# Kernel optimization log

Measured on AMD Instinct MI355X. Metric: run time of the kernel, lower is better.

The kernel has to match this reference:

```python
import jax, jax.numpy as jnp
import numpy as np


def setup_inputs() -> dict:
    key = jax.random.key(0)
    k1, k2, k3 = jax.random.split(key, 3)
    shape = (8, 2, 1024, 1024)
    predict = jax.random.normal(k1, shape, dtype=jnp.float32)
    target = jax.random.normal(k2, shape, dtype=jnp.float32)
    weight = jax.random.uniform(k3, shape, dtype=jnp.float32)
    return {"predict": predict, "target": target, "weight": weight, "min_kept": 2000000}


def reference(predict, target, weight, min_kept):
    # norm_term = prod(spatial dims) * batch  (channels NOT included, per source)
    B = predict.shape[0]
    spatial = float(np.prod(predict.shape[2:]))
    norm_term = jnp.float32(spatial * B)

    sq = (predict - target) ** 2
    loss_flat = (sq / norm_term).reshape(-1)          # unweighted per-elem MSE
    # threshold = sorted_ascending[N - min_kept] == min_kept-th largest value.
    # top_k replaces the full sort (same order statistic, ties identical).
    topk_vals, _ = jax.lax.top_k(loss_flat, min_kept)
    threshold = topk_vals[min_kept - 1]

    wloss_flat = (weight * sq / norm_term).reshape(-1)
    mask = loss_flat > threshold                      # strict >, as in source
    cnt = jnp.sum(mask)
    # reduction == 'elementwise_mean': mean over selected elements
    return jnp.sum(jnp.where(mask, wloss_flat, 0.0)) / cnt.astype(wloss_flat.dtype)
```

## Files before the change

### kernel.cpp

```cpp
#include <hip/hip_runtime.h>
#include <stdint.h>


#define H2_BITS 17
#define H1_SIZE 32768
#define H1_WORDS (H1_SIZE / 2)
#define H2_SIZE 131072
#define SHARDS 64

#define OFF_H2   262144
#define OFF_META 786432
#define OFF_SUMS 786496
#define OFF_SHC  786560
#define OFF_CAND 786944

__device__ __forceinline__ void hist_add4(uint32_t* lh, float4 pv, float4 tv) {
    float d0 = pv.x - tv.x, d1 = pv.y - tv.y, d2 = pv.z - tv.z, d3 = pv.w - tv.w;
    uint32_t b0 = __float_as_uint(d0 * d0 * 0x1p-23f) >> H2_BITS;
    uint32_t b1 = __float_as_uint(d1 * d1 * 0x1p-23f) >> H2_BITS;
    uint32_t b2 = __float_as_uint(d2 * d2 * 0x1p-23f) >> H2_BITS;
    uint32_t b3 = __float_as_uint(d3 * d3 * 0x1p-23f) >> H2_BITS;
    atomicAdd(&lh[b0 >> 1], 1u << ((b0 & 1) * 16));
    atomicAdd(&lh[b1 >> 1], 1u << ((b1 & 1) * 16));
    atomicAdd(&lh[b2 >> 1], 1u << ((b2 & 1) * 16));
    atomicAdd(&lh[b3 >> 1], 1u << ((b3 & 1) * 16));
}

__global__ __launch_bounds__(1024) void k_hist1(
    const float4* __restrict__ p, const float4* __restrict__ t,
    uint32_t* __restrict__ hist1, int n4)
{
    __shared__ uint32_t lh[H1_WORDS];
    for (int j = threadIdx.x; j < H1_WORDS; j += 1024) lh[j] = 0;
    __syncthreads();
    const int S = gridDim.x * 1024;
    int i = blockIdx.x * 1024 + threadIdx.x;
    for (; i + 3 * S < n4; i += 4 * S) {
        float4 pv0 = p[i],         tv0 = t[i];
        float4 pv1 = p[i + S],     tv1 = t[i + S];
        float4 pv2 = p[i + 2 * S], tv2 = t[i + 2 * S];
        float4 pv3 = p[i + 3 * S], tv3 = t[i + 3 * S];
        hist_add4(lh, pv0, tv0);
        hist_add4(lh, pv1, tv1);
        hist_add4(lh, pv2, tv2);
        hist_add4(lh, pv3, tv3);
    }
    for (; i < n4; i += S) hist_add4(lh, p[i], t[i]);
    __syncthreads();
    uint32_t* dst = hist1 + (blockIdx.x & 1) * H1_SIZE;
    const uint32_t rot = (blockIdx.x >> 1) * 64;
    for (int jj = threadIdx.x; jj < H1_WORDS; jj += 1024) {
        int j = (int)((jj + rot) & (H1_WORDS - 1));
        uint32_t v = lh[j];
        uint32_t c0 = v & 0xFFFFu, c1 = v >> 16;
        if (c0) atomicAdd(&dst[2 * j], c0);
        if (c1) atomicAdd(&dst[2 * j + 1], c1);
    }
}

__global__ __launch_bounds__(1024) void k_scan1(
    const uint32_t* __restrict__ hist1, const int* __restrict__ min_kept,
    uint32_t* __restrict__ meta)
{
    __shared__ uint32_t psum[1024];
    __shared__ uint32_t gsuf[64];
    const int t = threadIdx.x;
    const uint32_t k = (uint32_t)(*min_kept);
    const uint32_t* h0 = hist1;
    const uint32_t* h1 = hist1 + H1_SIZE;
    const int per = H1_SIZE / 1024;
    const int base = t * per;
    uint32_t s = 0;
    #pragma unroll
    for (int i = 0; i < per; i++) s += h0[base + i] + h1[base + i];
    psum[t] = s;
    __syncthreads();
    if (t < 64) {
        uint32_t g = 0;
        for (int i = 0; i < 16; i++) g += psum[t * 16 + i];
        uint32_t v = g;
        #pragma unroll
        for (int off = 1; off < 64; off <<= 1) {
            uint32_t o = __shfl_down(v, off);
            if (t + off < 64) v += o;
        }
        gsuf[t] = v;
    }
    __syncthreads();
    const int g = t >> 4;
    uint32_t cum = (g < 63) ? gsuf[g + 1] : 0;
    const int gend = g * 16 + 15;
    for (int j = t + 1; j <= gend; j++) cum += psum[j];
    if (cum < k && k <= cum + psum[t]) {
        uint32_t c = cum;
        for (int i = per - 1; i >= 0; i--) {
            uint32_t h = h0[base + i] + h1[base + i];
            c += h;
            if (c >= k) {
                meta[0] = (uint32_t)(base + i);
                meta[1] = k - (c - h);
                break;
            }
        }
    }
}

__global__ __launch_bounds__(256) void k_main(
    const float4* __restrict__ p, const float4* __restrict__ t,
    const float4* __restrict__ w,
    uint32_t* meta, uint32_t* __restrict__ hist2,
    double* __restrict__ sums, uint32_t* __restrict__ shard_cnt,
    uint2* __restrict__ cand, uint32_t cap_per_shard, int n4)
{
    const uint32_t b = meta[0];
    double lsum = 0.0;
    uint32_t lcnt = 0;
    const int shard = blockIdx.x & (SHARDS - 1);
    uint32_t* my_cnt = &shard_cnt[shard];
    uint2* my_cand = cand + (size_t)shard * cap_per_shard;
    const int lane = threadIdx.x & 63;

    auto proc = [&](float4 pv, float4 tv, float4 wv) {
        float d[4] = {pv.x - tv.x, pv.y - tv.y, pv.z - tv.z, pv.w - tv.w};
        float wa[4] = {wv.x, wv.y, wv.z, wv.w};
        #pragma unroll
        for (int c = 0; c < 4; c++) {
            float loss = d[c] * d[c] * 0x1p-23f;
            uint32_t bits = __float_as_uint(loss);
            uint32_t hi = bits >> H2_BITS;
            if (hi > b) {
                lcnt++;
                lsum += (double)(wa[c] * loss);
            }
            unsigned long long m = __ballot(hi == b);
            if (m) {
                if (hi == b) {
                    int pos = __popcll(m & ((1ull << lane) - 1ull));
                    int leader = __ffsll(m) - 1;
                    uint32_t base_ = 0;
                    if (lane == leader)
                        base_ = atomicAdd(my_cnt, (uint32_t)__popcll(m));
                    base_ = __shfl(base_, leader);
                    uint32_t idx = base_ + (uint32_t)pos;
                    if (idx < cap_per_shard)
                        my_cand[idx] = make_uint2(bits, __float_as_uint(wa[c]));
                    else
                        meta[3] = 1u;
                    atomicAdd(&hist2[bits & (H2_SIZE - 1)], 1u);
                }
            }
        }
    };

    const int S = gridDim.x * 256;
    int i = blockIdx.x * 256 + threadIdx.x;
    for (; i + S < n4; i += 2 * S) {
        float4 pv0 = p[i],     tv0 = t[i],     wv0 = w[i];
        float4 pv1 = p[i + S], tv1 = t[i + S], wv1 = w[i + S];
        proc(pv0, tv0, wv0);
        proc(pv1, tv1, wv1);
    }
    for (; i < n4; i += S) proc(p[i], t[i], w[i]);

    #pragma unroll
    for (int off = 32; off; off >>= 1) {
        lsum += __shfl_down(lsum, off);
        lcnt += __shfl_down(lcnt, off);
    }
    __shared__ double sred[4];
    __shared__ uint32_t cred[4];
    const int wid = threadIdx.x >> 6;
    if (lane == 0) { sred[wid] = lsum; cred[wid] = lcnt; }
    __syncthreads();
    if (threadIdx.x == 0) {
        double bs = sred[0] + sred[1] + sred[2] + sred[3];
        uint32_t bc = cred[0] + cred[1] + cred[2] + cred[3];
        atomicAdd(&sums[0], bs);
        atomicAdd(&meta[4], bc);
    }
}

__global__ __launch_bounds__(1024) void k_scan2(
    const uint32_t* __restrict__ hist2, uint32_t* meta)
{
    __shared__ uint32_t psum[1024];
    __shared__ uint32_t gsuf[64];
    const int t = threadIdx.x;
    const uint32_t k = meta[1];
    const uint32_t b = meta[0];
    const int per = H2_SIZE / 1024;
    const int base = t * per;
    uint32_t s = 0;
    for (int i = 0; i < per; i++) s += hist2[base + i];
    psum[t] = s;
    __syncthreads();
    if (t < 64) {
        uint32_t g = 0;
        for (int i = 0; i < 16; i++) g += psum[t * 16 + i];
        uint32_t v = g;
        #pragma unroll
        for (int off = 1; off < 64; off <<= 1) {
            uint32_t o = __shfl_down(v, off);
            if (t + off < 64) v += o;
        }
        gsuf[t] = v;
    }
    __syncthreads();
    const int g = t >> 4;
    uint32_t cum = (g < 63) ? gsuf[g + 1] : 0;
    const int gend = g * 16 + 15;
    for (int j = t + 1; j <= gend; j++) cum += psum[j];
    if (cum < k && k <= cum + psum[t]) {
        uint32_t c = cum;
        for (int i = per - 1; i >= 0; i--) {
            uint32_t h = hist2[base + i];
            c += h;
            if (c >= k) {
                meta[2] = (b << H2_BITS) | (uint32_t)(base + i);
                break;
            }
        }
    }
}

__global__ __launch_bounds__(256) void k_cand(
    const float4* __restrict__ p, const float4* __restrict__ t,
    const float4* __restrict__ w,
    uint32_t* meta, const uint32_t* __restrict__ shard_cnt,
    const uint2* __restrict__ cand, uint32_t cap_per_shard,
    double* __restrict__ sums, int n4)
{
    const uint32_t thr = meta[2];
    const uint32_t overflow = meta[3];
    double lsum = 0.0;
    uint32_t lcnt = 0;
    if (!overflow) {
        for (int sdx = 0; sdx < SHARDS; sdx++) {
            uint32_t cnt = shard_cnt[sdx];
            if (cnt > cap_per_shard) cnt = cap_per_shard;
            const uint2* cs = cand + (size_t)sdx * cap_per_shard;
            for (uint32_t i = blockIdx.x * 256 + threadIdx.x; i < cnt;
                 i += gridDim.x * 256) {
                uint2 e = cs[i];
                if (e.x > thr) {
                    lcnt++;
                    lsum += (double)(__uint_as_float(e.y) * __uint_as_float(e.x));
                }
            }
        }
    } else {
        const uint32_t bb = meta[0];
        const int S = gridDim.x * 256;
        for (int i = blockIdx.x * 256 + threadIdx.x; i < n4; i += S) {
            float4 pv = p[i], tv = t[i], wv = w[i];
            float d[4] = {pv.x - tv.x, pv.y - tv.y, pv.z - tv.z, pv.w - tv.w};
            float wa[4] = {wv.x, wv.y, wv.z, wv.w};
            #pragma unroll
            for (int c = 0; c < 4; c++) {
                float loss = d[c] * d[c] * 0x1p-23f;
                uint32_t bits = __float_as_uint(loss);
                if ((bits >> H2_BITS) == bb && bits > thr) {
                    lcnt++;
                    lsum += (double)(wa[c] * loss);
                }
            }
        }
    }
    #pragma unroll
    for (int off = 32; off; off >>= 1) {
        lsum += __shfl_down(lsum, off);
        lcnt += __shfl_down(lcnt, off);
    }
    __shared__ double sred[4];
    __shared__ uint32_t cred[4];
    const int wid = threadIdx.x >> 6, lane = threadIdx.x & 63;
    if (lane == 0) { sred[wid] = lsum; cred[wid] = lcnt; }
    __syncthreads();
    if (threadIdx.x == 0) {
        double bs = sred[0] + sred[1] + sred[2] + sred[3];
        uint32_t bc = cred[0] + cred[1] + cred[2] + cred[3];
        atomicAdd(&sums[1], bs);
        atomicAdd(&meta[5], bc);
    }
}

__global__ __launch_bounds__(64) void k_final(
    const double* __restrict__ sums, const uint32_t* __restrict__ meta,
    float* __restrict__ out)
{
    if (threadIdx.x == 0 && blockIdx.x == 0) {
        double s = sums[0] + sums[1];
        double c = (double)(meta[4] + meta[5]);
        out[0] = (float)(s / c);
    }
}

extern "C" void kernel_launch(void* const* d_in, const int* in_sizes, int n_in,
                              void* d_out, int out_size, void* d_ws, size_t ws_size,
                              hipStream_t stream) {
    const float* p = (const float*)d_in[0];
    const float* t = (const float*)d_in[1];
    const float* w = (const float*)d_in[2];
    const int* mk = (const int*)d_in[3];
    float* out = (float*)d_out;
    const int n = in_sizes[0];
    const int n4 = n / 4;

    uint8_t* ws = (uint8_t*)d_ws;
    uint32_t* hist1 = (uint32_t*)ws;
    uint32_t* hist2 = (uint32_t*)(ws + OFF_H2);
    uint32_t* meta  = (uint32_t*)(ws + OFF_META);
    double*   sums  = (double*)(ws + OFF_SUMS);
    uint32_t* shcnt = (uint32_t*)(ws + OFF_SHC);
    uint2*    cand  = (uint2*)(ws + OFF_CAND);
    uint32_t cap_per_shard = 0;
    if (ws_size > OFF_CAND + SHARDS * 8) {
        cap_per_shard = (uint32_t)((ws_size - OFF_CAND) / (8 * SHARDS));
    }

    hipMemsetAsync(d_ws, 0, OFF_CAND, stream);
    k_hist1<<<512, 1024, 0, stream>>>((const float4*)p, (const float4*)t, hist1, n4);
    k_scan1<<<1, 1024, 0, stream>>>(hist1, mk, meta);
    k_main<<<2048, 256, 0, stream>>>((const float4*)p, (const float4*)t,
                                     (const float4*)w, meta, hist2, sums, shcnt,
                                     cand, cap_per_shard, n4);
    k_scan2<<<1, 1024, 0, stream>>>(hist2, meta);
    k_cand<<<256, 256, 0, stream>>>((const float4*)p, (const float4*)t,
                                    (const float4*)w, meta, shcnt, cand,
                                    cap_per_shard, sums, n4);
    k_final<<<1, 64, 0, stream>>>(sums, meta, out);
}
```

Baseline: 386.1 us.

## Software-pipeline streaming loads and move hist2 build into separate candidate kernel

The histogram and main passes switch from grid-stride loops to fixed contiguous chunks per block (8192 and 4096 float4s). Loads are explicitly pipelined ahead of compute, with scheduling barriers keeping several loads in flight. The main kernel drops the per-wave ballot and the sharded candidate counters in favour of one global atomic counter per candidate element. Building the second-level histogram moves into a new small kernel that reads the candidate list, so the main streaming pass does less atomic work. In exchange it adds a kernel launch and risks contention on the single global counter if many elements fall in the threshold bucket.

```diff
diff --git a/kernel.cpp b/kernel.cpp
--- a/kernel.cpp
+++ b/kernel.cpp
@@ -6,13 +6,13 @@
 #define H1_SIZE 32768
 #define H1_WORDS (H1_SIZE / 2)
 #define H2_SIZE 131072
-#define SHARDS 64
 
 #define OFF_H2   262144
 #define OFF_META 786432
 #define OFF_SUMS 786496
-#define OFF_SHC  786560
-#define OFF_CAND 786944
+#define OFF_CAND 786560
+
+#define SB() __builtin_amdgcn_sched_barrier(0)
 
 __device__ __forceinline__ void hist_add4(uint32_t* lh, float4 pv, float4 tv) {
     float d0 = pv.x - tv.x, d1 = pv.y - tv.y, d2 = pv.z - tv.z, d3 = pv.w - tv.w;
@@ -33,19 +33,26 @@
     __shared__ uint32_t lh[H1_WORDS];
     for (int j = threadIdx.x; j < H1_WORDS; j += 1024) lh[j] = 0;
     __syncthreads();
-    const int S = gridDim.x * 1024;
-    int i = blockIdx.x * 1024 + threadIdx.x;
-    for (; i + 3 * S < n4; i += 4 * S) {
-        float4 pv0 = p[i],         tv0 = t[i];
-        float4 pv1 = p[i + S],     tv1 = t[i + S];
-        float4 pv2 = p[i + 2 * S], tv2 = t[i + 2 * S];
-        float4 pv3 = p[i + 3 * S], tv3 = t[i + 3 * S];
-        hist_add4(lh, pv0, tv0);
-        hist_add4(lh, pv1, tv1);
-        hist_add4(lh, pv2, tv2);
-        hist_add4(lh, pv3, tv3);
-    }
-    for (; i < n4; i += S) hist_add4(lh, p[i], t[i]);
+    const int tid = threadIdx.x;
+    const int base = blockIdx.x * 8192;
+    if (base + 8192 <= n4) {
+        const float4* pb = p + base;
+        const float4* tb = t + base;
+#define H1LD(u) float4 P##u = pb[tid + (u)*1024]; float4 T##u = tb[tid + (u)*1024];
+#define H1PR(u) hist_add4(lh, P##u, T##u);
+        H1LD(0) H1LD(1) H1LD(2)
+        SB();
+        H1LD(3) SB(); H1PR(0)
+        H1LD(4) SB(); H1PR(1)
+        H1LD(5) SB(); H1PR(2)
+        H1LD(6) SB(); H1PR(3)
+        H1LD(7) SB(); H1PR(4)
+        H1PR(5) H1PR(6) H1PR(7)
+#undef H1LD
+#undef H1PR
+    } else {
+        for (int i = base + tid; i < n4; i += 1024) hist_add4(lh, p[i], t[i]);
+    }
     __syncthreads();
     uint32_t* dst = hist1 + (blockIdx.x & 1) * H1_SIZE;
     const uint32_t rot = (blockIdx.x >> 1) * 64;
@@ -107,60 +114,66 @@
 
 __global__ __launch_bounds__(256) void k_main(
     const float4* __restrict__ p, const float4* __restrict__ t,
-    const float4* __restrict__ w,
-    uint32_t* meta, uint32_t* __restrict__ hist2,
-    double* __restrict__ sums, uint32_t* __restrict__ shard_cnt,
-    uint2* __restrict__ cand, uint32_t cap_per_shard, int n4)
+    const float4* __restrict__ w, uint32_t* meta,
+    double* __restrict__ sums, uint2* __restrict__ cand,
+    uint32_t cap, int n4)
 {
     const uint32_t b = meta[0];
     double lsum = 0.0;
     uint32_t lcnt = 0;
-    const int shard = blockIdx.x & (SHARDS - 1);
-    uint32_t* my_cnt = &shard_cnt[shard];
-    uint2* my_cand = cand + (size_t)shard * cap_per_shard;
-    const int lane = threadIdx.x & 63;
+    const int tid = threadIdx.x;
+    const int base = blockIdx.x * 4096;
 
     auto proc = [&](float4 pv, float4 tv, float4 wv) {
-        float d[4] = {pv.x - tv.x, pv.y - tv.y, pv.z - tv.z, pv.w - tv.w};
+        float d0 = pv.x - tv.x, d1 = pv.y - tv.y, d2 = pv.z - tv.z, d3 = pv.w - tv.w;
+        float l0 = d0 * d0 * 0x1p-23f, l1 = d1 * d1 * 0x1p-23f;
+        float l2 = d2 * d2 * 0x1p-23f, l3 = d3 * d3 * 0x1p-23f;
         float wa[4] = {wv.x, wv.y, wv.z, wv.w};
+        float lo[4] = {l0, l1, l2, l3};
         #pragma unroll
         for (int c = 0; c < 4; c++) {
-            float loss = d[c] * d[c] * 0x1p-23f;
-            uint32_t bits = __float_as_uint(loss);
+            uint32_t bits = __float_as_uint(lo[c]);
             uint32_t hi = bits >> H2_BITS;
-            if (hi > b) {
-                lcnt++;
-                lsum += (double)(wa[c] * loss);
-            }
-            unsigned long long m = __ballot(hi == b);
-            if (m) {
-                if (hi == b) {
-                    int pos = __popcll(m & ((1ull << lane) - 1ull));
-                    int leader = __ffsll(m) - 1;
-                    uint32_t base_ = 0;
-                    if (lane == leader)
-                        base_ = atomicAdd(my_cnt, (uint32_t)__popcll(m));
-                    base_ = __shfl(base_, leader);
-                    uint32_t idx = base_ + (uint32_t)pos;
-                    if (idx < cap_per_shard)
-                        my_cand[idx] = make_uint2(bits, __float_as_uint(wa[c]));
-                    else
-                        meta[3] = 1u;
-                    atomicAdd(&hist2[bits & (H2_SIZE - 1)], 1u);
-                }
+            bool above = hi > b;
+            lcnt += above ? 1u : 0u;
+            lsum += above ? (double)(wa[c] * lo[c]) : 0.0;
+            if (hi == b) {
+                uint32_t idx = atomicAdd(&meta[6], 1u);
+                if (idx < cap) cand[idx] = make_uint2(bits, __float_as_uint(wa[c]));
+                else meta[3] = 1u;
             }
         }
     };
 
-    const int S = gridDim.x * 256;
-    int i = blockIdx.x * 256 + threadIdx.x;
-    for (; i + S < n4; i += 2 * S) {
-        float4 pv0 = p[i],     tv0 = t[i],     wv0 = w[i];
-        float4 pv1 = p[i + S], tv1 = t[i + S], wv1 = w[i + S];
-        proc(pv0, tv0, wv0);
-        proc(pv1, tv1, wv1);
-    }
-    for (; i < n4; i += S) proc(p[i], t[i], w[i]);
+    if (base + 4096 <= n4) {
+        const float4* pb = p + base;
+        const float4* tb = t + base;
+        const float4* wb = w + base;
+#define MLD(u) float4 P##u = pb[tid + (u)*256]; float4 T##u = tb[tid + (u)*256]; \
+               float4 W##u = wb[tid + (u)*256];
+#define MPR(u) proc(P##u, T##u, W##u);
+        MLD(0) MLD(1)
+        SB();
+        MLD(2)  SB(); MPR(0)
+        MLD(3)  SB(); MPR(1)
+        MLD(4)  SB(); MPR(2)
+        MLD(5)  SB(); MPR(3)
+        MLD(6)  SB(); MPR(4)
+        MLD(7)  SB(); MPR(5)
+        MLD(8)  SB(); MPR(6)
+        MLD(9)  SB(); MPR(7)
+        MLD(10) SB(); MPR(8)
+        MLD(11) SB(); MPR(9)
+        MLD(12) SB(); MPR(10)
+        MLD(13) SB(); MPR(11)
+        MLD(14) SB(); MPR(12)
+        MLD(15) SB(); MPR(13)
+        MPR(14) MPR(15)
+#undef MLD
+#undef MPR
+    } else {
+        for (int i = base + tid; i < n4; i += 256) proc(p[i], t[i], w[i]);
+    }
 
     #pragma unroll
     for (int off = 32; off; off >>= 1) {
@@ -169,7 +182,7 @@
     }
     __shared__ double sred[4];
     __shared__ uint32_t cred[4];
-    const int wid = threadIdx.x >> 6;
+    const int wid = threadIdx.x >> 6, lane = threadIdx.x & 63;
     if (lane == 0) { sred[wid] = lsum; cred[wid] = lcnt; }
     __syncthreads();
     if (threadIdx.x == 0) {
@@ -177,6 +190,34 @@
         uint32_t bc = cred[0] + cred[1] + cred[2] + cred[3];
         atomicAdd(&sums[0], bs);
         atomicAdd(&meta[4], bc);
+    }
+}
+
+__global__ __launch_bounds__(256) void k_hist2b(
+    const float4* __restrict__ p, const float4* __restrict__ t,
+    uint32_t* __restrict__ meta, const uint2* __restrict__ cand,
+    uint32_t cap, uint32_t* __restrict__ hist2, int n4)
+{
+    if (!meta[3]) {
+        uint32_t cnt = meta[6];
+        if (cnt > cap) cnt = cap;
+        for (uint32_t i = blockIdx.x * 256 + threadIdx.x; i < cnt;
+             i += gridDim.x * 256) {
+            atomicAdd(&hist2[cand[i].x & (H2_SIZE - 1)], 1u);
+        }
+    } else {
+        const uint32_t b = meta[0];
+        const int S = gridDim.x * 256;
+        for (int i = blockIdx.x * 256 + threadIdx.x; i < n4; i += S) {
+            float4 pv = p[i], tv = t[i];
+            float d[4] = {pv.x - tv.x, pv.y - tv.y, pv.z - tv.z, pv.w - tv.w};
+            #pragma unroll
+            for (int c = 0; c < 4; c++) {
+                uint32_t bits = __float_as_uint(d[c] * d[c] * 0x1p-23f);
+                if ((bits >> H2_BITS) == b)
+                    atomicAdd(&hist2[bits & (H2_SIZE - 1)], 1u);
+            }
+        }
     }
 }
 
@@ -225,9 +266,8 @@
 
 __global__ __launch_bounds__(256) void k_cand(
     const float4* __restrict__ p, const float4* __restrict__ t,
-    const float4* __restrict__ w,
-    uint32_t* meta, const uint32_t* __restrict__ shard_cnt,
-    const uint2* __restrict__ cand, uint32_t cap_per_shard,
+    const float4* __restrict__ w, uint32_t* meta,
+    const uint2* __restrict__ cand, uint32_t cap,
     double* __restrict__ sums, int n4)
 {
     const uint32_t thr = meta[2];
@@ -235,17 +275,14 @@
     double lsum = 0.0;
     uint32_t lcnt = 0;
     if (!overflow) {
-        for (int sdx = 0; sdx < SHARDS; sdx++) {
-            uint32_t cnt = shard_cnt[sdx];
-            if (cnt > cap_per_shard) cnt = cap_per_shard;
-            const uint2* cs = cand + (size_t)sdx * cap_per_shard;
-            for (uint32_t i = blockIdx.x * 256 + threadIdx.x; i < cnt;
-                 i += gridDim.x * 256) {
-                uint2 e = cs[i];
-                if (e.x > thr) {
-                    lcnt++;
-                    lsum += (double)(__uint_as_float(e.y) * __uint_as_float(e.x));
-                }
+        uint32_t cnt = meta[6];
+        if (cnt > cap) cnt = cap;
+        for (uint32_t i = blockIdx.x * 256 + threadIdx.x; i < cnt;
+             i += gridDim.x * 256) {
+            uint2 e = cand[i];
+            if (e.x > thr) {
+                lcnt++;
+                lsum += (double)(__uint_as_float(e.y) * __uint_as_float(e.x));
             }
         }
     } else {
@@ -311,22 +348,23 @@
     uint32_t* hist2 = (uint32_t*)(ws + OFF_H2);
     uint32_t* meta  = (uint32_t*)(ws + OFF_META);
     double*   sums  = (double*)(ws + OFF_SUMS);
-    uint32_t* shcnt = (uint32_t*)(ws + OFF_SHC);
     uint2*    cand  = (uint2*)(ws + OFF_CAND);
-    uint32_t cap_per_shard = 0;
-    if (ws_size > OFF_CAND + SHARDS * 8) {
-        cap_per_shard = (uint32_t)((ws_size - OFF_CAND) / (8 * SHARDS));
+    uint32_t cap = 0;
+    if (ws_size > OFF_CAND + 8) {
+        cap = (uint32_t)((ws_size - OFF_CAND) / 8);
     }
 
     hipMemsetAsync(d_ws, 0, OFF_CAND, stream);
-    k_hist1<<<512, 1024, 0, stream>>>((const float4*)p, (const float4*)t, hist1, n4);
+    const int nb1 = (n4 + 8191) / 8192;
+    const int nbm = (n4 + 4095) / 4096;
+    k_hist1<<<nb1, 1024, 0, stream>>>((const float4*)p, (const float4*)t, hist1, n4);
     k_scan1<<<1, 1024, 0, stream>>>(hist1, mk, meta);
-    k_main<<<2048, 256, 0, stream>>>((const float4*)p, (const float4*)t,
-                                     (const float4*)w, meta, hist2, sums, shcnt,
-                                     cand, cap_per_shard, n4);
+    k_main<<<nbm, 256, 0, stream>>>((const float4*)p, (const float4*)t,
+                                    (const float4*)w, meta, sums, cand, cap, n4);
+    k_hist2b<<<32, 256, 0, stream>>>((const float4*)p, (const float4*)t,
+                                     meta, cand, cap, hist2, n4);
     k_scan2<<<1, 1024, 0, stream>>>(hist2, meta);
-    k_cand<<<256, 256, 0, stream>>>((const float4*)p, (const float4*)t,
-                                    (const float4*)w, meta, shcnt, cand,
-                                    cap_per_shard, sums, n4);
+    k_cand<<<64, 256, 0, stream>>>((const float4*)p, (const float4*)t,
+                                   (const float4*)w, meta, cand, cap, sums, n4);
     k_final<<<1, 64, 0, stream>>>(sums, meta, out);
 }
```

Result: slower. 681.4 us (+76.5%).

## Replace full-pass histogram with sampled bounds and candidate-window selection

Applied to the files above, without the earlier changes.

Replaces the full first-pass histogram over predict/target with a small strided sample (64 blocks, 2 chunks per wave) that estimates a bin window bracketing the k-th largest loss. The main pass then accumulates elements above the window and collects in-window candidates, and later histogram/scan stages run only on those candidates. A fallback path redoes full histograms over the data if the window guess is wrong or the buffer overflows. The 1/norm scale is dropped from the per-element loss and applied once at the end. This removes one full read of two inputs but adds several small serial kernel launches.

```diff
diff --git a/kernel.cpp b/kernel.cpp
--- a/kernel.cpp
+++ b/kernel.cpp
@@ -2,77 +2,70 @@
 #include <stdint.h>
 
 
-#define H2_BITS 17
-#define H1_SIZE 32768
-#define H1_WORDS (H1_SIZE / 2)
+#define BIN_SHIFT 17
+#define NBINS 32768
+#define NB_WORDS (NBINS / 2)
+#define WMAX 4096
 #define H2_SIZE 131072
 #define SHARDS 64
 
-#define OFF_H2   262144
-#define OFF_META 786432
-#define OFF_SUMS 786496
-#define OFF_SHC  786560
-#define OFF_CAND 786944
+#define OFF_WIN   131072u
+#define OFF_H2    147456u
+#define OFF_FULL  671744u
+#define OFF_META  802816u
+#define OFF_SUMS  802944u
+#define OFF_SHC   802976u
+#define OFF_CAND  803232u
 
 __device__ __forceinline__ void hist_add4(uint32_t* lh, float4 pv, float4 tv) {
     float d0 = pv.x - tv.x, d1 = pv.y - tv.y, d2 = pv.z - tv.z, d3 = pv.w - tv.w;
-    uint32_t b0 = __float_as_uint(d0 * d0 * 0x1p-23f) >> H2_BITS;
-    uint32_t b1 = __float_as_uint(d1 * d1 * 0x1p-23f) >> H2_BITS;
-    uint32_t b2 = __float_as_uint(d2 * d2 * 0x1p-23f) >> H2_BITS;
-    uint32_t b3 = __float_as_uint(d3 * d3 * 0x1p-23f) >> H2_BITS;
+    uint32_t b0 = __float_as_uint(d0 * d0) >> BIN_SHIFT;
+    uint32_t b1 = __float_as_uint(d1 * d1) >> BIN_SHIFT;
+    uint32_t b2 = __float_as_uint(d2 * d2) >> BIN_SHIFT;
+    uint32_t b3 = __float_as_uint(d3 * d3) >> BIN_SHIFT;
     atomicAdd(&lh[b0 >> 1], 1u << ((b0 & 1) * 16));
     atomicAdd(&lh[b1 >> 1], 1u << ((b1 & 1) * 16));
     atomicAdd(&lh[b2 >> 1], 1u << ((b2 & 1) * 16));
     atomicAdd(&lh[b3 >> 1], 1u << ((b3 & 1) * 16));
 }
 
-__global__ __launch_bounds__(1024) void k_hist1(
+__global__ __launch_bounds__(256) void k_sample(
     const float4* __restrict__ p, const float4* __restrict__ t,
-    uint32_t* __restrict__ hist1, int n4)
-{
-    __shared__ uint32_t lh[H1_WORDS];
-    for (int j = threadIdx.x; j < H1_WORDS; j += 1024) lh[j] = 0;
-    __syncthreads();
-    const int S = gridDim.x * 1024;
-    int i = blockIdx.x * 1024 + threadIdx.x;
-    for (; i + 3 * S < n4; i += 4 * S) {
-        float4 pv0 = p[i],         tv0 = t[i];
-        float4 pv1 = p[i + S],     tv1 = t[i + S];
-        float4 pv2 = p[i + 2 * S], tv2 = t[i + 2 * S];
-        float4 pv3 = p[i + 3 * S], tv3 = t[i + 3 * S];
-        hist_add4(lh, pv0, tv0);
-        hist_add4(lh, pv1, tv1);
-        hist_add4(lh, pv2, tv2);
-        hist_add4(lh, pv3, tv3);
-    }
-    for (; i < n4; i += S) hist_add4(lh, p[i], t[i]);
-    __syncthreads();
-    uint32_t* dst = hist1 + (blockIdx.x & 1) * H1_SIZE;
-    const uint32_t rot = (blockIdx.x >> 1) * 64;
-    for (int jj = threadIdx.x; jj < H1_WORDS; jj += 1024) {
-        int j = (int)((jj + rot) & (H1_WORDS - 1));
+    uint32_t* __restrict__ shist, int n4, int chunk_stride)
+{
+    __shared__ uint32_t lh[NB_WORDS];
+    for (int j = threadIdx.x; j < NB_WORDS; j += 256) lh[j] = 0;
+    __syncthreads();
+    const int gw = blockIdx.x * 4 + (threadIdx.x >> 6);
+    const int lane = threadIdx.x & 63;
+    #pragma unroll
+    for (int c = 0; c < 2; c++) {
+        int ch = gw * 2 + c;
+        int idx = ch * chunk_stride + lane;
+        if (idx < n4) hist_add4(lh, p[idx], t[idx]);
+    }
+    __syncthreads();
+    for (int j = threadIdx.x; j < NB_WORDS; j += 256) {
         uint32_t v = lh[j];
         uint32_t c0 = v & 0xFFFFu, c1 = v >> 16;
-        if (c0) atomicAdd(&dst[2 * j], c0);
-        if (c1) atomicAdd(&dst[2 * j + 1], c1);
-    }
-}
-
-__global__ __launch_bounds__(1024) void k_scan1(
-    const uint32_t* __restrict__ hist1, const int* __restrict__ min_kept,
-    uint32_t* __restrict__ meta)
+        if (c0) atomicAdd(&shist[2 * j], c0);
+        if (c1) atomicAdd(&shist[2 * j + 1], c1);
+    }
+}
+
+__global__ __launch_bounds__(1024) void k_bounds(
+    const uint32_t* __restrict__ shist, const int* __restrict__ mk,
+    uint32_t* __restrict__ meta, uint32_t inv)
 {
     __shared__ uint32_t psum[1024];
     __shared__ uint32_t gsuf[64];
+    __shared__ uint32_t sBh, sBlp1;
     const int t = threadIdx.x;
-    const uint32_t k = (uint32_t)(*min_kept);
-    const uint32_t* h0 = hist1;
-    const uint32_t* h1 = hist1 + H1_SIZE;
-    const int per = H1_SIZE / 1024;
+    if (t == 0) { sBh = 0xFFFFFFFFu; sBlp1 = 0u; }
+    const int per = NBINS / 1024;
     const int base = t * per;
     uint32_t s = 0;
-    #pragma unroll
-    for (int i = 0; i < per; i++) s += h0[base + i] + h1[base + i];
+    for (int i = 0; i < per; i++) s += shist[base + i];
     psum[t] = s;
     __syncthreads();
     if (t < 64) {
@@ -91,62 +84,83 @@
     uint32_t cum = (g < 63) ? gsuf[g + 1] : 0;
     const int gend = g * 16 + 15;
     for (int j = t + 1; j <= gend; j++) cum += psum[j];
-    if (cum < k && k <= cum + psum[t]) {
-        uint32_t c = cum;
-        for (int i = per - 1; i >= 0; i--) {
-            uint32_t h = h0[base + i] + h1[base + i];
-            c += h;
-            if (c >= k) {
-                meta[0] = (uint32_t)(base + i);
-                meta[1] = k - (c - h);
-                break;
-            }
-        }
+
+    const uint32_t k = (uint32_t)(*mk);
+    const uint32_t M = k / 25 + inv;
+    const uint32_t A = (k > M) ? (k - M) / inv : 0u;
+    const uint32_t B = (k + M + inv - 1) / inv;
+    uint32_t srun = cum;
+    uint32_t lminBh = 0xFFFFFFFFu, lmaxBl = 0u;
+    for (int i = per - 1; i >= 0; i--) {
+        uint32_t j = (uint32_t)(base + i);
+        if (srun <= A) lminBh = j;
+        if (srun >= B && lmaxBl == 0u) lmaxBl = j + 1;
+        srun += shist[base + i];
+    }
+    if (lminBh != 0xFFFFFFFFu) atomicMin(&sBh, lminBh);
+    if (lmaxBl) atomicMax(&sBlp1, lmaxBl);
+    __syncthreads();
+    if (t == 0) {
+        int bh = (sBh == 0xFFFFFFFFu) ? (NBINS - 1) : (int)sBh;
+        int bl = (int)sBlp1 - 1;
+        if (bl >= bh) bl = bh - 1;
+        if (bh - bl > WMAX) bl = bh - WMAX;
+        meta[0] = (uint32_t)bl;
+        meta[1] = (uint32_t)bh;
     }
 }
 
 __global__ __launch_bounds__(256) void k_main(
     const float4* __restrict__ p, const float4* __restrict__ t,
-    const float4* __restrict__ w,
-    uint32_t* meta, uint32_t* __restrict__ hist2,
+    const float4* __restrict__ w, uint32_t* __restrict__ meta,
     double* __restrict__ sums, uint32_t* __restrict__ shard_cnt,
-    uint2* __restrict__ cand, uint32_t cap_per_shard, int n4)
-{
-    const uint32_t b = meta[0];
+    uint2* __restrict__ cand, uint32_t cap, int n4)
+{
+    const int bl = (int)meta[0];
+    const int bh = (int)meta[1];
     double lsum = 0.0;
     uint32_t lcnt = 0;
+    const int lane = threadIdx.x & 63;
     const int shard = blockIdx.x & (SHARDS - 1);
     uint32_t* my_cnt = &shard_cnt[shard];
-    uint2* my_cand = cand + (size_t)shard * cap_per_shard;
-    const int lane = threadIdx.x & 63;
+    uint2* my_cand = cand + (size_t)shard * cap;
 
     auto proc = [&](float4 pv, float4 tv, float4 wv) {
-        float d[4] = {pv.x - tv.x, pv.y - tv.y, pv.z - tv.z, pv.w - tv.w};
-        float wa[4] = {wv.x, wv.y, wv.z, wv.w};
-        #pragma unroll
-        for (int c = 0; c < 4; c++) {
-            float loss = d[c] * d[c] * 0x1p-23f;
-            uint32_t bits = __float_as_uint(loss);
-            uint32_t hi = bits >> H2_BITS;
-            if (hi > b) {
-                lcnt++;
-                lsum += (double)(wa[c] * loss);
-            }
-            unsigned long long m = __ballot(hi == b);
-            if (m) {
-                if (hi == b) {
-                    int pos = __popcll(m & ((1ull << lane) - 1ull));
-                    int leader = __ffsll(m) - 1;
+        float d0 = pv.x - tv.x, d1 = pv.y - tv.y, d2 = pv.z - tv.z, d3 = pv.w - tv.w;
+        float s0 = d0 * d0, s1 = d1 * d1, s2 = d2 * d2, s3 = d3 * d3;
+        uint32_t q0 = __float_as_uint(s0), q1 = __float_as_uint(s1);
+        uint32_t q2 = __float_as_uint(s2), q3 = __float_as_uint(s3);
+        int e0 = (int)(q0 >> BIN_SHIFT), e1 = (int)(q1 >> BIN_SHIFT);
+        int e2 = (int)(q2 >> BIN_SHIFT), e3 = (int)(q3 >> BIN_SHIFT);
+        bool a0 = e0 > bh, a1 = e1 > bh, a2 = e2 > bh, a3 = e3 > bh;
+        lcnt += (a0 ? 1u : 0u) + (a1 ? 1u : 0u) + (a2 ? 1u : 0u) + (a3 ? 1u : 0u);
+        lsum += a0 ? (double)(wv.x * s0) : 0.0;
+        lsum += a1 ? (double)(wv.y * s1) : 0.0;
+        lsum += a2 ? (double)(wv.z * s2) : 0.0;
+        lsum += a3 ? (double)(wv.w * s3) : 0.0;
+        bool c0 = (!a0) && (e0 > bl), c1 = (!a1) && (e1 > bl);
+        bool c2 = (!a2) && (e2 > bl), c3 = (!a3) && (e3 > bl);
+        if (__ballot(c0 | c1 | c2 | c3)) {
+            uint32_t qs[4] = {q0, q1, q2, q3};
+            float wws[4] = {wv.x, wv.y, wv.z, wv.w};
+            bool cs[4] = {c0, c1, c2, c3};
+            #pragma unroll
+            for (int c = 0; c < 4; c++) {
+                unsigned long long m = __ballot(cs[c]);
+                if (m) {
+                    int leader = __ffsll((unsigned long long)m) - 1;
                     uint32_t base_ = 0;
                     if (lane == leader)
                         base_ = atomicAdd(my_cnt, (uint32_t)__popcll(m));
                     base_ = __shfl(base_, leader);
-                    uint32_t idx = base_ + (uint32_t)pos;
-                    if (idx < cap_per_shard)
-                        my_cand[idx] = make_uint2(bits, __float_as_uint(wa[c]));
-                    else
-                        meta[3] = 1u;
-                    atomicAdd(&hist2[bits & (H2_SIZE - 1)], 1u);
+                    if (cs[c]) {
+                        uint32_t idx = base_ +
+                            (uint32_t)__popcll(m & ((1ull << lane) - 1ull));
+                        if (idx < cap)
+                            my_cand[idx] = make_uint2(qs[c], __float_as_uint(wws[c]));
+                        else
+                            meta[3] = 1u;
+                    }
                 }
             }
         }
@@ -173,25 +187,76 @@
     if (lane == 0) { sred[wid] = lsum; cred[wid] = lcnt; }
     __syncthreads();
     if (threadIdx.x == 0) {
-        double bs = sred[0] + sred[1] + sred[2] + sred[3];
-        uint32_t bc = cred[0] + cred[1] + cred[2] + cred[3];
-        atomicAdd(&sums[0], bs);
-        atomicAdd(&meta[4], bc);
-    }
-}
-
-__global__ __launch_bounds__(1024) void k_scan2(
-    const uint32_t* __restrict__ hist2, uint32_t* meta)
+        atomicAdd(&sums[0], sred[0] + sred[1] + sred[2] + sred[3]);
+        atomicAdd(&meta[4], cred[0] + cred[1] + cred[2] + cred[3]);
+    }
+}
+
+__global__ __launch_bounds__(64) void k_check(
+    const uint32_t* __restrict__ shc, const int* __restrict__ mk,
+    uint32_t* __restrict__ meta)
+{
+    uint32_t c = shc[threadIdx.x];
+    #pragma unroll
+    for (int off = 32; off; off >>= 1) c += __shfl_down(c, off);
+    if (threadIdx.x == 0) {
+        uint32_t k = (uint32_t)(*mk);
+        uint32_t cntA = meta[4];
+        int bl = (int)meta[0], bh = (int)meta[1];
+        uint32_t W = (uint32_t)(bh - bl);
+        bool ok = (meta[3] == 0u) && (cntA < k) && (k <= cntA + c) &&
+                  (W >= 1u) && (W <= (uint32_t)WMAX);
+        meta[2] = ok ? 0u : 2u;
+        meta[5] = c;
+        meta[11] = ok ? (k - cntA) : 0u;
+    }
+}
+
+__global__ __launch_bounds__(256) void k_winhist(
+    const float4* __restrict__ p, const float4* __restrict__ t,
+    const uint32_t* __restrict__ shc, const uint2* __restrict__ cand,
+    uint32_t cap, uint32_t* __restrict__ meta,
+    uint32_t* __restrict__ winhist, uint32_t* __restrict__ fullhist, int n4)
+{
+    if (meta[2] == 0u) {
+        __shared__ uint32_t lw[WMAX];
+        for (int j = threadIdx.x; j < WMAX; j += 256) lw[j] = 0;
+        __syncthreads();
+        const int bl = (int)meta[0];
+        const int s = blockIdx.x;
+        if (s < SHARDS) {
+            uint32_t cnt = shc[s]; if (cnt > cap) cnt = cap;
+            const uint2* cs = cand + (size_t)s * cap;
+            for (uint32_t i = threadIdx.x; i < cnt; i += 256) {
+                int wi = (int)(cs[i].x >> BIN_SHIFT) - bl - 1;
+                atomicAdd(&lw[wi], 1u);
+            }
+        }
+        __syncthreads();
+        for (int j = threadIdx.x; j < WMAX; j += 256)
+            if (lw[j]) atomicAdd(&winhist[j], lw[j]);
+    } else {
+        const int S = gridDim.x * 256;
+        for (int i = blockIdx.x * 256 + threadIdx.x; i < n4; i += S) {
+            float4 pv = p[i], tv = t[i];
+            float d[4] = {pv.x - tv.x, pv.y - tv.y, pv.z - tv.z, pv.w - tv.w};
+            #pragma unroll
+            for (int c = 0; c < 4; c++)
+                atomicAdd(&fullhist[__float_as_uint(d[c] * d[c]) >> BIN_SHIFT], 1u);
+        }
+    }
+}
+
+__device__ void suffix_select(const uint32_t* __restrict__ h, int per,
+                              uint32_t r, uint32_t* out2)
 {
     __shared__ uint32_t psum[1024];
     __shared__ uint32_t gsuf[64];
     const int t = threadIdx.x;
-    const uint32_t k = meta[1];
-    const uint32_t b = meta[0];
-    const int per = H2_SIZE / 1024;
+    if (t == 0) { out2[0] = 0u; out2[1] = 1u; }
     const int base = t * per;
     uint32_t s = 0;
-    for (int i = 0; i < per; i++) s += hist2[base + i];
+    for (int i = 0; i < per; i++) s += h[base + i];
     psum[t] = s;
     __syncthreads();
     if (t < 64) {
@@ -210,46 +275,100 @@
     uint32_t cum = (g < 63) ? gsuf[g + 1] : 0;
     const int gend = g * 16 + 15;
     for (int j = t + 1; j <= gend; j++) cum += psum[j];
-    if (cum < k && k <= cum + psum[t]) {
+    if (cum < r && r <= cum + psum[t]) {
         uint32_t c = cum;
         for (int i = per - 1; i >= 0; i--) {
-            uint32_t h = hist2[base + i];
-            c += h;
-            if (c >= k) {
-                meta[2] = (b << H2_BITS) | (uint32_t)(base + i);
+            uint32_t hh = h[base + i];
+            c += hh;
+            if (c >= r) {
+                out2[0] = (uint32_t)(base + i);
+                out2[1] = r - (c - hh);
                 break;
             }
         }
     }
-}
-
-__global__ __launch_bounds__(256) void k_cand(
+    __syncthreads();
+}
+
+__global__ __launch_bounds__(1024) void k2_scan(
+    const uint32_t* __restrict__ winhist, const uint32_t* __restrict__ fullhist,
+    const int* __restrict__ mk, uint32_t* __restrict__ meta)
+{
+    __shared__ uint32_t out2[2];
+    const uint32_t mode = meta[2];
+    const uint32_t* src = mode ? fullhist : winhist;
+    const int per = mode ? (NBINS / 1024) : (WMAX / 1024);
+    const uint32_t r = mode ? (uint32_t)(*mk) : meta[11];
+    suffix_select(src, per, r, out2);
+    if (threadIdx.x == 0) {
+        uint32_t b = mode ? out2[0]
+                          : (uint32_t)((int)meta[0] + 1 + (int)out2[0]);
+        meta[6] = b;
+        meta[7] = out2[1];
+    }
+}
+
+__global__ __launch_bounds__(256) void k3_hist(
     const float4* __restrict__ p, const float4* __restrict__ t,
-    const float4* __restrict__ w,
-    uint32_t* meta, const uint32_t* __restrict__ shard_cnt,
-    const uint2* __restrict__ cand, uint32_t cap_per_shard,
-    double* __restrict__ sums, int n4)
-{
-    const uint32_t thr = meta[2];
-    const uint32_t overflow = meta[3];
+    const uint32_t* __restrict__ shc, const uint2* __restrict__ cand,
+    uint32_t cap, uint32_t* __restrict__ meta, uint32_t* __restrict__ hist2,
+    int n4)
+{
+    const uint32_t b = meta[6];
+    if (meta[2] == 0u) {
+        const int s = blockIdx.x;
+        if (s >= SHARDS) return;
+        uint32_t cnt = shc[s]; if (cnt > cap) cnt = cap;
+        const uint2* cs = cand + (size_t)s * cap;
+        for (uint32_t i = threadIdx.x; i < cnt; i += 256) {
+            uint32_t q = cs[i].x;
+            if ((q >> BIN_SHIFT) == b) atomicAdd(&hist2[q & (H2_SIZE - 1)], 1u);
+        }
+    } else {
+        const int S = gridDim.x * 256;
+        for (int i = blockIdx.x * 256 + threadIdx.x; i < n4; i += S) {
+            float4 pv = p[i], tv = t[i];
+            float d[4] = {pv.x - tv.x, pv.y - tv.y, pv.z - tv.z, pv.w - tv.w};
+            #pragma unroll
+            for (int c = 0; c < 4; c++) {
+                uint32_t q = __float_as_uint(d[c] * d[c]);
+                if ((q >> BIN_SHIFT) == b) atomicAdd(&hist2[q & (H2_SIZE - 1)], 1u);
+            }
+        }
+    }
+}
+
+__global__ __launch_bounds__(1024) void k3_scan(
+    const uint32_t* __restrict__ hist2, uint32_t* __restrict__ meta)
+{
+    __shared__ uint32_t out2[2];
+    suffix_select(hist2, H2_SIZE / 1024, meta[7], out2);
+    if (threadIdx.x == 0)
+        meta[8] = (meta[6] << BIN_SHIFT) | out2[0];
+}
+
+__global__ __launch_bounds__(256) void k4_sum(
+    const float4* __restrict__ p, const float4* __restrict__ t,
+    const float4* __restrict__ w, const uint32_t* __restrict__ shc,
+    const uint2* __restrict__ cand, uint32_t cap,
+    uint32_t* __restrict__ meta, double* __restrict__ sums, int n4)
+{
+    const uint32_t thr = meta[8];
     double lsum = 0.0;
     uint32_t lcnt = 0;
-    if (!overflow) {
-        for (int sdx = 0; sdx < SHARDS; sdx++) {
-            uint32_t cnt = shard_cnt[sdx];
-            if (cnt > cap_per_shard) cnt = cap_per_shard;
-            const uint2* cs = cand + (size_t)sdx * cap_per_shard;
-            for (uint32_t i = blockIdx.x * 256 + threadIdx.x; i < cnt;
-                 i += gridDim.x * 256) {
-                uint2 e = cs[i];
-                if (e.x > thr) {
-                    lcnt++;
-                    lsum += (double)(__uint_as_float(e.y) * __uint_as_float(e.x));
-                }
+    if (meta[2] == 0u) {
+        const int s = blockIdx.x & (SHARDS - 1);
+        uint32_t cnt = shc[s]; if (cnt > cap) cnt = cap;
+        const uint2* cs = cand + (size_t)s * cap;
+        for (uint32_t i = (blockIdx.x >> 6) * 256 + threadIdx.x; i < cnt;
+             i += (gridDim.x >> 6) * 256) {
+            uint2 e = cs[i];
+            if (e.x > thr) {
+                lcnt++;
+                lsum += (double)(__uint_as_float(e.y) * __uint_as_float(e.x));
             }
         }
     } else {
-        const uint32_t bb = meta[0];
         const int S = gridDim.x * 256;
         for (int i = blockIdx.x * 256 + threadIdx.x; i < n4; i += S) {
             float4 pv = p[i], tv = t[i], wv = w[i];
@@ -257,11 +376,10 @@
             float wa[4] = {wv.x, wv.y, wv.z, wv.w};
             #pragma unroll
             for (int c = 0; c < 4; c++) {
-                float loss = d[c] * d[c] * 0x1p-23f;
-                uint32_t bits = __float_as_uint(loss);
-                if ((bits >> H2_BITS) == bb && bits > thr) {
+                float sq = d[c] * d[c];
+                if (__float_as_uint(sq) > thr) {
                     lcnt++;
-                    lsum += (double)(wa[c] * loss);
+                    lsum += (double)(wa[c] * sq);
                 }
             }
         }
@@ -277,10 +395,8 @@
     if (lane == 0) { sred[wid] = lsum; cred[wid] = lcnt; }
     __syncthreads();
     if (threadIdx.x == 0) {
-        double bs = sred[0] + sred[1] + sred[2] + sred[3];
-        uint32_t bc = cred[0] + cred[1] + cred[2] + cred[3];
-        atomicAdd(&sums[1], bs);
-        atomicAdd(&meta[5], bc);
+        atomicAdd(&sums[1], sred[0] + sred[1] + sred[2] + sred[3]);
+        atomicAdd(&meta[9], cred[0] + cred[1] + cred[2] + cred[3]);
     }
 }
 
@@ -289,44 +405,55 @@
     float* __restrict__ out)
 {
     if (threadIdx.x == 0 && blockIdx.x == 0) {
-        double s = sums[0] + sums[1];
-        double c = (double)(meta[4] + meta[5]);
-        out[0] = (float)(s / c);
+        double s, c;
+        if (meta[2] == 0u) {
+            s = sums[0] + sums[1];
+            c = (double)(meta[4] + meta[9]);
+        } else {
+            s = sums[1];
+            c = (double)meta[9];
+        }
+        out[0] = (float)((s * 0x1p-23) / c);
     }
 }
 
 extern "C" void kernel_launch(void* const* d_in, const int* in_sizes, int n_in,
                               void* d_out, int out_size, void* d_ws, size_t ws_size,
                               hipStream_t stream) {
-    const float* p = (const float*)d_in[0];
-    const float* t = (const float*)d_in[1];
-    const float* w = (const float*)d_in[2];
+    const float4* p = (const float4*)d_in[0];
+    const float4* t = (const float4*)d_in[1];
+    const float4* w = (const float4*)d_in[2];
     const int* mk = (const int*)d_in[3];
     float* out = (float*)d_out;
     const int n = in_sizes[0];
     const int n4 = n / 4;
 
     uint8_t* ws = (uint8_t*)d_ws;
-    uint32_t* hist1 = (uint32_t*)ws;
-    uint32_t* hist2 = (uint32_t*)(ws + OFF_H2);
-    uint32_t* meta  = (uint32_t*)(ws + OFF_META);
-    double*   sums  = (double*)(ws + OFF_SUMS);
-    uint32_t* shcnt = (uint32_t*)(ws + OFF_SHC);
-    uint2*    cand  = (uint2*)(ws + OFF_CAND);
-    uint32_t cap_per_shard = 0;
-    if (ws_size > OFF_CAND + SHARDS * 8) {
-        cap_per_shard = (uint32_t)((ws_size - OFF_CAND) / (8 * SHARDS));
-    }
+    uint32_t* shist    = (uint32_t*)ws;
+    uint32_t* winhist  = (uint32_t*)(ws + OFF_WIN);
+    uint32_t* hist2    = (uint32_t*)(ws + OFF_H2);
+    uint32_t* fullhist = (uint32_t*)(ws + OFF_FULL);
+    uint32_t* meta     = (uint32_t*)(ws + OFF_META);
+    double*   sums     = (double*)(ws + OFF_SUMS);
+    uint32_t* shc      = (uint32_t*)(ws + OFF_SHC);
+    uint2*    cand     = (uint2*)(ws + OFF_CAND);
+    uint32_t cap = 0;
+    if (ws_size > OFF_CAND + 8ull * SHARDS)
+        cap = (uint32_t)((ws_size - OFF_CAND) / (8ull * SHARDS));
+
+    int chunk_stride = n4 / 512; if (chunk_stride < 1) chunk_stride = 1;
+    uint32_t inv = (uint32_t)(n / 131072); if (inv < 1) inv = 1;
 
     hipMemsetAsync(d_ws, 0, OFF_CAND, stream);
-    k_hist1<<<512, 1024, 0, stream>>>((const float4*)p, (const float4*)t, hist1, n4);
-    k_scan1<<<1, 1024, 0, stream>>>(hist1, mk, meta);
-    k_main<<<2048, 256, 0, stream>>>((const float4*)p, (const float4*)t,
-                                     (const float4*)w, meta, hist2, sums, shcnt,
-                                     cand, cap_per_shard, n4);
-    k_scan2<<<1, 1024, 0, stream>>>(hist2, meta);
-    k_cand<<<256, 256, 0, stream>>>((const float4*)p, (const float4*)t,
-                                    (const float4*)w, meta, shcnt, cand,
-                                    cap_per_shard, sums, n4);
+    k_sample<<<64, 256, 0, stream>>>(p, t, shist, n4, chunk_stride);
+    k_bounds<<<1, 1024, 0, stream>>>(shist, mk, meta, inv);
+    k_main<<<4096, 256, 0, stream>>>(p, t, w, meta, sums, shc, cand, cap, n4);
+    k_check<<<1, 64, 0, stream>>>(shc, mk, meta);
+    k_winhist<<<64, 256, 0, stream>>>(p, t, shc, cand, cap, meta, winhist,
+                                      fullhist, n4);
+    k2_scan<<<1, 1024, 0, stream>>>(winhist, fullhist, mk, meta);
+    k3_hist<<<64, 256, 0, stream>>>(p, t, shc, cand, cap, meta, hist2, n4);
+    k3_scan<<<1, 1024, 0, stream>>>(hist2, meta);
+    k4_sum<<<256, 256, 0, stream>>>(p, t, w, shc, cand, cap, meta, sums, n4);
     k_final<<<1, 64, 0, stream>>>(sums, meta, out);
 }
```

Measured after the change: 698.5 us. +80.9%, slower.
